# Kernel tuning notes

Measured on AMD Instinct MI355X. Metric: run time of the kernel, lower is better.

## Reference

```python
import jax, jax.numpy as jnp
import numpy as np

B, T, IN, H, L = 256, 80, 39, 256, 5


def _xavier(key, shape):
    fan_out, fan_in = shape[0], shape[1]
    std = (2.0 / (fan_in + fan_out)) ** 0.5
    return std * jax.random.normal(key, shape, dtype=jnp.float32)


def setup_inputs() -> dict:
    key = jax.random.key(0)
    ks = jax.random.split(key, 4 + 2 * L)
    x = jax.random.normal(ks[0], (B, T, IN), dtype=jnp.float32)
    # PyTorch LSTM params, gate order (i, f, g, o); biases zero per init.
    W_ih0 = _xavier(ks[1], (4 * H, IN))                       # layer 0 input weights
    W_ih_rest = jnp.stack([_xavier(ks[2 + l], (4 * H, H)) for l in range(L - 1)])  # [L-1,4H,H]
    W_hh = jnp.stack([_xavier(ks[1 + L + l], (4 * H, H)) for l in range(L)])       # [L,4H,H]
    b_ih = jnp.zeros((L, 4 * H), dtype=jnp.float32)
    b_hh = jnp.zeros((L, 4 * H), dtype=jnp.float32)
    fc_w = _xavier(ks[2 * L + 1], (1, H))
    fc_b = jnp.zeros((1,), dtype=jnp.float32)
    return {"x": x, "W_ih0": W_ih0, "W_ih_rest": W_ih_rest, "W_hh": W_hh,
            "b_ih": b_ih, "b_hh": b_hh, "fc_w": fc_w, "fc_b": fc_b}


def _lstm_layer(xs, W_ih, W_hh_l, b_ih_l, b_hh_l):
    # xs: [B,T,D]. Precompute input projection for all timesteps (one big GEMM).
    x_proj = jnp.einsum('btd,gd->btg', xs, W_ih) + b_ih_l + b_hh_l  # [B,T,4H]

    def step(carry, xp):
        h, c = carry
        gates = xp + h @ W_hh_l.T                 # [B,4H]
        i, f, g, o = jnp.split(gates, 4, axis=-1)
        c = jax.nn.sigmoid(f) * c + jax.nn.sigmoid(i) * jnp.tanh(g)
        h = jax.nn.sigmoid(o) * jnp.tanh(c)
        return (h, c), h

    b = xs.shape[0]
    h0 = jnp.zeros((b, H), dtype=xs.dtype)
    _, hs = jax.lax.scan(step, (h0, h0), jnp.swapaxes(x_proj, 0, 1))
    return jnp.swapaxes(hs, 0, 1)  # [B,T,H]


def reference(x, W_ih0, W_ih_rest, W_hh, b_ih, b_hh, fc_w, fc_b):
    h = _lstm_layer(x, W_ih0, W_hh[0], b_ih[0], b_hh[0])
    for l in range(1, L):
        h = _lstm_layer(h, W_ih_rest[l - 1], W_hh[l], b_ih[l], b_hh[l])
    out = jnp.einsum('bth,oh->bto', h, fc_w) + fc_b  # [B,T,1]
    return out[..., 0]  # [B,T]
```

## Files before the change

kernel.cpp:

```cpp
#include <hip/hip_runtime.h>

#define B_ 256
#define T_ 80
#define IN_ 39
#define H_ 256
#define G_ 1024
#define L_ 5
#define TC_ 16
#define NCH_ 5

#define XP_FLOATS   (B_ * TC_ * G_)
#define HBUF_FLOATS (B_ * T_ * H_)
#define CBUF_FLOATS (B_ * H_)
#define WG_FLOATS   (L_ * G_ * H_)
#define HX_FLOATS   (2 * 32 * 2048)
#define CNT_OFF_FLOATS (XP_FLOATS + HBUF_FLOATS + CBUF_FLOATS + WG_FLOATS + HX_FLOATS)

#define AG __HIP_MEMORY_SCOPE_AGENT

__device__ __forceinline__ float sigm(float x) { return 1.0f / (1.0f + expf(-x)); }
__device__ __forceinline__ void fma4(float4& a, float s, const float4& w) {
    a.x = fmaf(s, w.x, a.x); a.y = fmaf(s, w.y, a.y);
    a.z = fmaf(s, w.z, a.z); a.w = fmaf(s, w.w, a.w);
}
__device__ __forceinline__ void red4(float4& a) {
    a.x += __shfl_xor(a.x, 32); a.y += __shfl_xor(a.y, 32);
    a.z += __shfl_xor(a.z, 32); a.w += __shfl_xor(a.w, 32);
}
__device__ __forceinline__ float lo32(unsigned long long v) { return __uint_as_float((unsigned)v); }
__device__ __forceinline__ float hi32(unsigned long long v) { return __uint_as_float((unsigned)(v >> 32)); }

extern "C" __global__ void __launch_bounds__(256)
wt_kernel(const float* __restrict__ Whh, float* __restrict__ Wg) {
    const int gid = blockIdx.x * 256 + threadIdx.x;
    const int g4 = gid & 3;
    const int j  = (gid >> 2) & 31;
    const int k  = (gid >> 7) & 255;
    const int s  = (gid >> 15) & 7;
    const int l  = gid >> 18;
    Wg[gid] = Whh[((size_t)(l * 1024 + g4 * 256 + s * 32 + j)) * 256 + k];
}

extern "C" __global__ void __launch_bounds__(256)
proj_kernel(const float* __restrict__ src, const float* __restrict__ Wih,
            const float* __restrict__ bihl, const float* __restrict__ bhhl,
            float* __restrict__ xp, int K, int t0) {
    __shared__ float As[16 * 68];
    __shared__ float Bs[16 * 68];
    const int tid = threadIdx.x;
    const int mt = blockIdx.x >> 4, nt = blockIdx.x & 15;
    const int tx = tid & 15, ty = tid >> 4;
    const int lr = tid >> 2, lc4 = (tid & 3) << 2;

    const int ar = mt * 64 + lr;
    const int ab = ar >> 4;
    const int at = t0 + (ar & 15);
    const float* arow = src + ((size_t)ab * T_ + at) * K;
    const float* brow = Wih + (size_t)(nt * 64 + lr) * K;

    float acc[4][4];
    #pragma unroll
    for (int i = 0; i < 4; ++i)
        #pragma unroll
        for (int j = 0; j < 4; ++j) acc[i][j] = 0.0f;

    for (int k0 = 0; k0 < K; k0 += 16) {
        __syncthreads();
        if (K == IN_) {
            #pragma unroll
            for (int i = 0; i < 4; ++i) {
                int k = k0 + lc4 + i;
                As[(lc4 + i) * 68 + lr] = (k < IN_) ? arow[k] : 0.0f;
                Bs[(lc4 + i) * 68 + lr] = (k < IN_) ? brow[k] : 0.0f;
            }
        } else {
            float4 av = *(const float4*)(arow + k0 + lc4);
            float4 bv = *(const float4*)(brow + k0 + lc4);
            As[(lc4 + 0) * 68 + lr] = av.x;
            As[(lc4 + 1) * 68 + lr] = av.y;
            As[(lc4 + 2) * 68 + lr] = av.z;
            As[(lc4 + 3) * 68 + lr] = av.w;
            Bs[(lc4 + 0) * 68 + lr] = bv.x;
            Bs[(lc4 + 1) * 68 + lr] = bv.y;
            Bs[(lc4 + 2) * 68 + lr] = bv.z;
            Bs[(lc4 + 3) * 68 + lr] = bv.w;
        }
        __syncthreads();
        #pragma unroll
        for (int kk = 0; kk < 16; ++kk) {
            float4 a4 = *(const float4*)&As[kk * 68 + ty * 4];
            float4 b4 = *(const float4*)&Bs[kk * 68 + tx * 4];
            acc[0][0] += a4.x * b4.x; acc[0][1] += a4.x * b4.y;
            acc[0][2] += a4.x * b4.z; acc[0][3] += a4.x * b4.w;
            acc[1][0] += a4.y * b4.x; acc[1][1] += a4.y * b4.y;
            acc[1][2] += a4.y * b4.z; acc[1][3] += a4.y * b4.w;
            acc[2][0] += a4.z * b4.x; acc[2][1] += a4.z * b4.y;
            acc[2][2] += a4.z * b4.z; acc[2][3] += a4.z * b4.w;
            acc[3][0] += a4.w * b4.x; acc[3][1] += a4.w * b4.y;
            acc[3][2] += a4.w * b4.z; acc[3][3] += a4.w * b4.w;
        }
    }
    const int col = nt * 64 + tx * 4;
    const float bs0 = bihl[col + 0] + bhhl[col + 0];
    const float bs1 = bihl[col + 1] + bhhl[col + 1];
    const float bs2 = bihl[col + 2] + bhhl[col + 2];
    const float bs3 = bihl[col + 3] + bhhl[col + 3];
    #pragma unroll
    for (int i = 0; i < 4; ++i) {
        const int row = mt * 64 + ty * 4 + i;
        float4 o;
        o.x = acc[i][0] + bs0; o.y = acc[i][1] + bs1;
        o.z = acc[i][2] + bs2; o.w = acc[i][3] + bs3;
        *(float4*)&xp[(size_t)row * G_ + col] = o;
    }
}

extern "C" __global__ void __launch_bounds__(256, 1)
rec2_kernel(const float* __restrict__ xp, const float* __restrict__ Wg_l,
            float* __restrict__ hbuf, float* __restrict__ cbuf,
            float* __restrict__ hx, int* __restrict__ cnt,
            int t0, int chkb, int first) {
    extern __shared__ float smem[];
    float* sW = smem;
    float* sH = smem + 32768;
    float* sP = smem + 34816;

    const int tid = threadIdx.x;
    const int bid = blockIdx.x;
    const int grp = bid & 31;
    const int s   = bid >> 5;
    const int jj  = tid & 31;
    const int ks  = tid >> 5;
    const int w   = tid >> 6;
    const int fb  = tid >> 5;
    const int fj  = tid & 31;
    const int bglob = grp * 8 + fb;
    const int unit  = s * 32 + fj;
    int* cnt_g = cnt + grp * 32;

    {
        const float4* Wgs = (const float4*)Wg_l + (size_t)s * 8192;
        float4* sW4 = (float4*)sW;
        #pragma unroll 4
        for (int i = tid; i < 8192; i += 256) sW4[i] = Wgs[i];
    }

    float creg = first ? 0.0f : cbuf[(size_t)bglob * H_ + unit];
    const float4* sW4 = (const float4*)sW;

    for (int tt = 0; tt < TC_; ++tt) {
        const int t = t0 + tt;

        if (tt == 0) {
            if (first) {
                for (int i = tid; i < 2048; i += 256) sH[i] = 0.0f;
            } else {
                const int u = tid;
                #pragma unroll
                for (int bb = 0; bb < 8; ++bb)
                    sH[u * 8 + bb] = hbuf[((size_t)(grp * 8 + bb) * T_ + (t0 - 1)) * H_ + u];
            }
        } else {
            if (tid == 0) {
                const int tgt = 8 * (chkb + tt);
                while (__hip_atomic_load(cnt_g, __ATOMIC_RELAXED, AG) < tgt)
                    __builtin_amdgcn_s_sleep(1);
            }
            __syncthreads();
            const unsigned long long* hs =
                (const unsigned long long*)(hx + (size_t)(((tt - 1) & 1) * 32 + grp) * 2048);
            const int u = tid;
            unsigned long long v0 = __hip_atomic_load(hs + u * 4 + 0, __ATOMIC_RELAXED, AG);
            unsigned long long v1 = __hip_atomic_load(hs + u * 4 + 1, __ATOMIC_RELAXED, AG);
            unsigned long long v2 = __hip_atomic_load(hs + u * 4 + 2, __ATOMIC_RELAXED, AG);
            unsigned long long v3 = __hip_atomic_load(hs + u * 4 + 3, __ATOMIC_RELAXED, AG);
            float4 fa, fbv;
            fa.x = lo32(v0); fa.y = hi32(v0); fa.z = lo32(v1); fa.w = hi32(v1);
            fbv.x = lo32(v2); fbv.y = hi32(v2); fbv.z = lo32(v3); fbv.w = hi32(v3);
            *(float4*)&sH[u * 8] = fa;
            *(float4*)&sH[u * 8 + 4] = fbv;
        }

        const size_t xrow = ((size_t)bglob * TC_ + tt) * G_ + unit;
        const float x0 = xp[xrow];
        const float x1 = xp[xrow + 256];
        const float x2 = xp[xrow + 512];
        const float x3 = xp[xrow + 768];

        __syncthreads();

        float4 a0 = {0,0,0,0}, a1 = {0,0,0,0}, a2 = {0,0,0,0}, a3 = {0,0,0,0};
        float4 a4 = {0,0,0,0}, a5 = {0,0,0,0}, a6 = {0,0,0,0}, a7 = {0,0,0,0};
        #pragma unroll 4
        for (int kk = 0; kk < 32; ++kk) {
            const int k = ks * 32 + kk;
            const float4 wv = sW4[k * 32 + jj];
            const float4 ha = *(const float4*)&sH[k * 8];
            const float4 hb = *(const float4*)&sH[k * 8 + 4];
            fma4(a0, ha.x, wv); fma4(a1, ha.y, wv);
            fma4(a2, ha.z, wv); fma4(a3, ha.w, wv);
            fma4(a4, hb.x, wv); fma4(a5, hb.y, wv);
            fma4(a6, hb.z, wv); fma4(a7, hb.w, wv);
        }
        red4(a0); red4(a1); red4(a2); red4(a3);
        red4(a4); red4(a5); red4(a6); red4(a7);
        if ((tid & 63) < 32) {
            float4* pp = (float4*)&sP[(w * 32 + jj) * 36];
            pp[0] = a0; pp[1] = a1; pp[2] = a2; pp[3] = a3;
            pp[4] = a4; pp[5] = a5; pp[6] = a6; pp[7] = a7;
        }
        __syncthreads();

        float4 g4;
        g4.x = x0; g4.y = x1; g4.z = x2; g4.w = x3;
        #pragma unroll
        for (int w2 = 0; w2 < 4; ++w2) {
            const float4 pw = *(const float4*)&sP[(w2 * 32 + fj) * 36 + fb * 4];
            g4.x += pw.x; g4.y += pw.y; g4.z += pw.z; g4.w += pw.w;
        }
        const float I = sigm(g4.x);
        const float F = sigm(g4.y);
        const float Gt = tanhf(g4.z);
        const float O = sigm(g4.w);
        creg = F * creg + I * Gt;
        const float hval = O * tanhf(creg);
        hbuf[((size_t)bglob * T_ + t) * H_ + unit] = hval;

        if (tt < TC_ - 1) {
            __hip_atomic_store(hx + (size_t)((tt & 1) * 32 + grp) * 2048 + unit * 8 + fb,
                               hval, __ATOMIC_RELAXED, AG);
            asm volatile("s_waitcnt vmcnt(0)" ::: "memory");
            __syncthreads();
            if (tid == 0)
                __hip_atomic_fetch_add(cnt_g, 1, __ATOMIC_RELAXED, AG);
        }
    }

    cbuf[(size_t)bglob * H_ + unit] = creg;
}

extern "C" __global__ void __launch_bounds__(128)
fc_kernel(const float* __restrict__ hbuf, const float* __restrict__ fcw,
          const float* __restrict__ fcb, float* __restrict__ out) {
    __shared__ float wsm[256];
    const int tid = threadIdx.x;
    const int b = blockIdx.x;
    if (tid < 64) ((float4*)wsm)[tid] = ((const float4*)fcw)[tid];
    __syncthreads();
    if (tid < T_) {
        const float4* h4p = (const float4*)(hbuf + ((size_t)b * T_ + tid) * H_);
        const float4* w4p = (const float4*)wsm;
        float acc = fcb[0];
        #pragma unroll 8
        for (int k4 = 0; k4 < 64; ++k4) {
            float4 h4 = h4p[k4], w4 = w4p[k4];
            acc += h4.x * w4.x + h4.y * w4.y + h4.z * w4.z + h4.w * w4.w;
        }
        out[b * T_ + tid] = acc;
    }
}

extern "C" void kernel_launch(void* const* d_in, const int* in_sizes, int n_in,
                              void* d_out, int out_size, void* d_ws, size_t ws_size,
                              hipStream_t stream) {
    (void)in_sizes; (void)n_in; (void)out_size; (void)ws_size;
    const float* x    = (const float*)d_in[0];
    const float* Wih0 = (const float*)d_in[1];
    const float* Wihr = (const float*)d_in[2];
    const float* Whh  = (const float*)d_in[3];
    const float* bih  = (const float*)d_in[4];
    const float* bhh  = (const float*)d_in[5];
    const float* fcw  = (const float*)d_in[6];
    const float* fcb  = (const float*)d_in[7];
    float* out = (float*)d_out;
    float* ws  = (float*)d_ws;

    float* xp   = ws;
    float* hbuf = ws + XP_FLOATS;
    float* cbuf = hbuf + HBUF_FLOATS;
    float* wg   = cbuf + CBUF_FLOATS;
    float* hx   = wg + WG_FLOATS;
    int*   cnt  = (int*)(ws + CNT_OFF_FLOATS);

    hipMemsetAsync(cnt, 0, 32 * 32 * sizeof(int), stream);
    hipLaunchKernelGGL(wt_kernel, dim3(WG_FLOATS / 256), dim3(256), 0, stream, Whh, wg);

    for (int l = 0; l < L_; ++l) {
        const int K = (l == 0) ? IN_ : H_;
        const float* src = (l == 0) ? x : hbuf;
        const float* Wih = (l == 0) ? Wih0 : (Wihr + (size_t)(l - 1) * G_ * H_);
        const float* Wg_l = wg + (size_t)l * (G_ * H_);
        for (int ch = 0; ch < NCH_; ++ch) {
            const int t0 = ch * TC_;
            const int chkb = (l * NCH_ + ch) * (TC_ - 1);
            hipLaunchKernelGGL(proj_kernel, dim3(1024), dim3(256), 0, stream,
                               src, Wih, bih + l * G_, bhh + l * G_, xp, K, t0);
            hipLaunchKernelGGL(rec2_kernel, dim3(256), dim3(256), 157696, stream,
                               xp, Wg_l, hbuf, cbuf, hx, cnt, t0, chkb, ch == 0 ? 1 : 0);
        }
    }
    hipLaunchKernelGGL(fc_kernel, dim3(B_), dim3(128), 0, stream, hbuf, fcw, fcb, out);
}
```

Measured before the change: 2.688 ms.

## Replace counter barrier with tagged 64-bit h exchange slots

Each hidden value is now published as a 64-bit word that packs the float with a step tag. Consumers spin on their own 8 slots until every tag matches, instead of waiting on a per-group atomic counter. This removes the waitcnt, the extra __syncthreads and the fetch_add on the producer side, and the single-thread wait plus block barrier on the consumer side. The cost is more polling traffic, since every thread repeatedly loads 8 words, and the exchange buffer doubles in size and must be zeroed at start.

```diff
diff --git a/kernel.cpp b/kernel.cpp
--- a/kernel.cpp
+++ b/kernel.cpp
@@ -13,8 +13,8 @@
 #define HBUF_FLOATS (B_ * T_ * H_)
 #define CBUF_FLOATS (B_ * H_)
 #define WG_FLOATS   (L_ * G_ * H_)
-#define HX_FLOATS   (2 * 32 * 2048)
-#define CNT_OFF_FLOATS (XP_FLOATS + HBUF_FLOATS + CBUF_FLOATS + WG_FLOATS + HX_FLOATS)
+#define HX_U64      (2 * 32 * 2048)
+#define HX_OFF_FLOATS (XP_FLOATS + HBUF_FLOATS + CBUF_FLOATS + WG_FLOATS)
 
 #define AG __HIP_MEMORY_SCOPE_AGENT
 
@@ -27,8 +27,6 @@
     a.x += __shfl_xor(a.x, 32); a.y += __shfl_xor(a.y, 32);
     a.z += __shfl_xor(a.z, 32); a.w += __shfl_xor(a.w, 32);
 }
-__device__ __forceinline__ float lo32(unsigned long long v) { return __uint_as_float((unsigned)v); }
-__device__ __forceinline__ float hi32(unsigned long long v) { return __uint_as_float((unsigned)(v >> 32)); }
 
 extern "C" __global__ void __launch_bounds__(256)
 wt_kernel(const float* __restrict__ Whh, float* __restrict__ Wg) {
@@ -118,8 +116,8 @@
 extern "C" __global__ void __launch_bounds__(256, 1)
 rec2_kernel(const float* __restrict__ xp, const float* __restrict__ Wg_l,
             float* __restrict__ hbuf, float* __restrict__ cbuf,
-            float* __restrict__ hx, int* __restrict__ cnt,
-            int t0, int chkb, int first) {
+            unsigned long long* __restrict__ hx,
+            int t0, int tagb, int first) {
     extern __shared__ float smem[];
     float* sW = smem;
     float* sH = smem + 32768;
@@ -136,7 +134,6 @@
     const int fj  = tid & 31;
     const int bglob = grp * 8 + fb;
     const int unit  = s * 32 + fj;
-    int* cnt_g = cnt + grp * 32;
 
     {
         const float4* Wgs = (const float4*)Wg_l + (size_t)s * 8192;
@@ -161,24 +158,24 @@
                     sH[u * 8 + bb] = hbuf[((size_t)(grp * 8 + bb) * T_ + (t0 - 1)) * H_ + u];
             }
         } else {
-            if (tid == 0) {
-                const int tgt = 8 * (chkb + tt);
-                while (__hip_atomic_load(cnt_g, __ATOMIC_RELAXED, AG) < tgt)
-                    __builtin_amdgcn_s_sleep(1);
+            const unsigned exp_tag = (unsigned)(tagb + tt - 1);
+            const unsigned long long* hs =
+                hx + (size_t)(((tt - 1) & 1) * 32 + grp) * 2048 + (size_t)tid * 8;
+            unsigned long long v[8];
+            for (;;) {
+                bool ok = true;
+                #pragma unroll
+                for (int b = 0; b < 8; ++b)
+                    v[b] = __hip_atomic_load(hs + b, __ATOMIC_RELAXED, AG);
+                #pragma unroll
+                for (int b = 0; b < 8; ++b)
+                    ok = ok && ((unsigned)(v[b] >> 32) == exp_tag);
+                if (ok) break;
+                __builtin_amdgcn_s_sleep(1);
             }
-            __syncthreads();
-            const unsigned long long* hs =
-                (const unsigned long long*)(hx + (size_t)(((tt - 1) & 1) * 32 + grp) * 2048);
-            const int u = tid;
-            unsigned long long v0 = __hip_atomic_load(hs + u * 4 + 0, __ATOMIC_RELAXED, AG);
-            unsigned long long v1 = __hip_atomic_load(hs + u * 4 + 1, __ATOMIC_RELAXED, AG);
-            unsigned long long v2 = __hip_atomic_load(hs + u * 4 + 2, __ATOMIC_RELAXED, AG);
-            unsigned long long v3 = __hip_atomic_load(hs + u * 4 + 3, __ATOMIC_RELAXED, AG);
-            float4 fa, fbv;
-            fa.x = lo32(v0); fa.y = hi32(v0); fa.z = lo32(v1); fa.w = hi32(v1);
-            fbv.x = lo32(v2); fbv.y = hi32(v2); fbv.z = lo32(v3); fbv.w = hi32(v3);
-            *(float4*)&sH[u * 8] = fa;
-            *(float4*)&sH[u * 8 + 4] = fbv;
+            #pragma unroll
+            for (int b = 0; b < 8; ++b)
+                sH[tid * 8 + b] = __uint_as_float((unsigned)v[b]);
         }
 
         const size_t xrow = ((size_t)bglob * TC_ + tt) * G_ + unit;
@@ -227,12 +224,11 @@
         hbuf[((size_t)bglob * T_ + t) * H_ + unit] = hval;
 
         if (tt < TC_ - 1) {
-            __hip_atomic_store(hx + (size_t)((tt & 1) * 32 + grp) * 2048 + unit * 8 + fb,
-                               hval, __ATOMIC_RELAXED, AG);
-            asm volatile("s_waitcnt vmcnt(0)" ::: "memory");
-            __syncthreads();
-            if (tid == 0)
-                __hip_atomic_fetch_add(cnt_g, 1, __ATOMIC_RELAXED, AG);
+            const unsigned long long pv =
+                ((unsigned long long)(unsigned)(tagb + tt) << 32) | __float_as_uint(hval);
+            __hip_atomic_store(hx + (size_t)((tt & 1) * 32 + grp) * 2048
+                                  + (size_t)unit * 8 + fb,
+                               pv, __ATOMIC_RELAXED, AG);
         }
     }
 
@@ -279,10 +275,9 @@
     float* hbuf = ws + XP_FLOATS;
     float* cbuf = hbuf + HBUF_FLOATS;
     float* wg   = cbuf + CBUF_FLOATS;
-    float* hx   = wg + WG_FLOATS;
-    int*   cnt  = (int*)(ws + CNT_OFF_FLOATS);
-
-    hipMemsetAsync(cnt, 0, 32 * 32 * sizeof(int), stream);
+    unsigned long long* hx = (unsigned long long*)(ws + HX_OFF_FLOATS);
+
+    hipMemsetAsync(hx, 0, HX_U64 * sizeof(unsigned long long), stream);
     hipLaunchKernelGGL(wt_kernel, dim3(WG_FLOATS / 256), dim3(256), 0, stream, Whh, wg);
 
     for (int l = 0; l < L_; ++l) {
@@ -292,11 +287,11 @@
         const float* Wg_l = wg + (size_t)l * (G_ * H_);
         for (int ch = 0; ch < NCH_; ++ch) {
             const int t0 = ch * TC_;
-            const int chkb = (l * NCH_ + ch) * (TC_ - 1);
+            const int tagb = (l * NCH_ + ch) * TC_ + 1;
             hipLaunchKernelGGL(proj_kernel, dim3(1024), dim3(256), 0, stream,
                                src, Wih, bih + l * G_, bhh + l * G_, xp, K, t0);
             hipLaunchKernelGGL(rec2_kernel, dim3(256), dim3(256), 157696, stream,
-                               xp, Wg_l, hbuf, cbuf, hx, cnt, t0, chkb, ch == 0 ? 1 : 0);
+                               xp, Wg_l, hbuf, cbuf, hx, t0, tagb, ch == 0 ? 1 : 0);
         }
     }
     hipLaunchKernelGGL(fc_kernel, dim3(B_), dim3(128), 0, stream, hbuf, fcw, fcb, out);
```

Result: slower. 3.940 ms (+46.6%).

## Keep recurrent weights in registers with 512-thread blocks instead of LDS

Applied to the files above, without the earlier changes.

The recurrent kernel now loads each thread's slice of W_hh into 16 float4 registers instead of staging 128KB in shared memory. Block size doubles to 512 threads, so each thread covers 16 k-values, and the cross-wave partial-sum reduction widens to 8 slices. Only the first 256 threads run the gate math. The aim is to remove LDS bandwidth pressure on the weight reads in the per-step matvec and to add more waves for latency hiding. In exchange, register pressure rises and the reduction step grows.

```diff
diff --git a/kernel.cpp b/kernel.cpp
--- a/kernel.cpp
+++ b/kernel.cpp
@@ -115,15 +115,13 @@
     }
 }
 
-extern "C" __global__ void __launch_bounds__(256, 1)
-rec2_kernel(const float* __restrict__ xp, const float* __restrict__ Wg_l,
+extern "C" __global__ void __launch_bounds__(512, 2)
+rec3_kernel(const float* __restrict__ xp, const float* __restrict__ Wg_l,
             float* __restrict__ hbuf, float* __restrict__ cbuf,
             float* __restrict__ hx, int* __restrict__ cnt,
             int t0, int chkb, int first) {
-    extern __shared__ float smem[];
-    float* sW = smem;
-    float* sH = smem + 32768;
-    float* sP = smem + 34816;
+    __shared__ float sH[2048];
+    __shared__ float sP[8 * 32 * 36];
 
     const int tid = threadIdx.x;
     const int bid = blockIdx.x;
@@ -132,29 +130,30 @@
     const int jj  = tid & 31;
     const int ks  = tid >> 5;
     const int w   = tid >> 6;
-    const int fb  = tid >> 5;
+    const int fb  = (tid >> 5) & 7;
     const int fj  = tid & 31;
     const int bglob = grp * 8 + fb;
     const int unit  = s * 32 + fj;
     int* cnt_g = cnt + grp * 32;
 
-    {
-        const float4* Wgs = (const float4*)Wg_l + (size_t)s * 8192;
-        float4* sW4 = (float4*)sW;
-        #pragma unroll 4
-        for (int i = tid; i < 8192; i += 256) sW4[i] = Wgs[i];
-    }
-
-    float creg = first ? 0.0f : cbuf[(size_t)bglob * H_ + unit];
-    const float4* sW4 = (const float4*)sW;
+    const float4* Wg4 = (const float4*)Wg_l + (size_t)s * 8192;
+    float4 wreg[16];
+    #pragma unroll
+    for (int kk = 0; kk < 16; ++kk)
+        wreg[kk] = Wg4[(size_t)(ks * 16 + kk) * 32 + jj];
+
+    float creg = 0.0f;
+    if (tid < 256 && !first) creg = cbuf[(size_t)bglob * H_ + unit];
+
+    const float4* sH4 = (const float4*)sH;
 
     for (int tt = 0; tt < TC_; ++tt) {
         const int t = t0 + tt;
 
         if (tt == 0) {
             if (first) {
-                for (int i = tid; i < 2048; i += 256) sH[i] = 0.0f;
-            } else {
+                for (int i = tid; i < 2048; i += 512) sH[i] = 0.0f;
+            } else if (tid < 256) {
                 const int u = tid;
                 #pragma unroll
                 for (int bb = 0; bb < 8; ++bb)
@@ -167,36 +166,41 @@
                     __builtin_amdgcn_s_sleep(1);
             }
             __syncthreads();
-            const unsigned long long* hs =
-                (const unsigned long long*)(hx + (size_t)(((tt - 1) & 1) * 32 + grp) * 2048);
-            const int u = tid;
-            unsigned long long v0 = __hip_atomic_load(hs + u * 4 + 0, __ATOMIC_RELAXED, AG);
-            unsigned long long v1 = __hip_atomic_load(hs + u * 4 + 1, __ATOMIC_RELAXED, AG);
-            unsigned long long v2 = __hip_atomic_load(hs + u * 4 + 2, __ATOMIC_RELAXED, AG);
-            unsigned long long v3 = __hip_atomic_load(hs + u * 4 + 3, __ATOMIC_RELAXED, AG);
-            float4 fa, fbv;
-            fa.x = lo32(v0); fa.y = hi32(v0); fa.z = lo32(v1); fa.w = hi32(v1);
-            fbv.x = lo32(v2); fbv.y = hi32(v2); fbv.z = lo32(v3); fbv.w = hi32(v3);
-            *(float4*)&sH[u * 8] = fa;
-            *(float4*)&sH[u * 8 + 4] = fbv;
-        }
-
-        const size_t xrow = ((size_t)bglob * TC_ + tt) * G_ + unit;
-        const float x0 = xp[xrow];
-        const float x1 = xp[xrow + 256];
-        const float x2 = xp[xrow + 512];
-        const float x3 = xp[xrow + 768];
+            if (tid < 256) {
+                const unsigned long long* hs =
+                    (const unsigned long long*)(hx + (size_t)(((tt - 1) & 1) * 32 + grp) * 2048);
+                const int u = tid;
+                unsigned long long v0 = __hip_atomic_load(hs + u * 4 + 0, __ATOMIC_RELAXED, AG);
+                unsigned long long v1 = __hip_atomic_load(hs + u * 4 + 1, __ATOMIC_RELAXED, AG);
+                unsigned long long v2 = __hip_atomic_load(hs + u * 4 + 2, __ATOMIC_RELAXED, AG);
+                unsigned long long v3 = __hip_atomic_load(hs + u * 4 + 3, __ATOMIC_RELAXED, AG);
+                float4 fa, fbv;
+                fa.x = lo32(v0); fa.y = hi32(v0); fa.z = lo32(v1); fa.w = hi32(v1);
+                fbv.x = lo32(v2); fbv.y = hi32(v2); fbv.z = lo32(v3); fbv.w = hi32(v3);
+                *(float4*)&sH[u * 8] = fa;
+                *(float4*)&sH[u * 8 + 4] = fbv;
+            }
+        }
+
+        float x0 = 0.f, x1 = 0.f, x2 = 0.f, x3 = 0.f;
+        if (tid < 256) {
+            const size_t xrow = ((size_t)bglob * TC_ + tt) * G_ + unit;
+            x0 = xp[xrow];
+            x1 = xp[xrow + 256];
+            x2 = xp[xrow + 512];
+            x3 = xp[xrow + 768];
+        }
 
         __syncthreads();
 
         float4 a0 = {0,0,0,0}, a1 = {0,0,0,0}, a2 = {0,0,0,0}, a3 = {0,0,0,0};
         float4 a4 = {0,0,0,0}, a5 = {0,0,0,0}, a6 = {0,0,0,0}, a7 = {0,0,0,0};
-        #pragma unroll 4
-        for (int kk = 0; kk < 32; ++kk) {
-            const int k = ks * 32 + kk;
-            const float4 wv = sW4[k * 32 + jj];
-            const float4 ha = *(const float4*)&sH[k * 8];
-            const float4 hb = *(const float4*)&sH[k * 8 + 4];
+        #pragma unroll
+        for (int kk = 0; kk < 16; ++kk) {
+            const int k = ks * 16 + kk;
+            const float4 wv = wreg[kk];
+            const float4 ha = sH4[k * 2];
+            const float4 hb = sH4[k * 2 + 1];
             fma4(a0, ha.x, wv); fma4(a1, ha.y, wv);
             fma4(a2, ha.z, wv); fma4(a3, ha.w, wv);
             fma4(a4, hb.x, wv); fma4(a5, hb.y, wv);
@@ -211,24 +215,29 @@
         }
         __syncthreads();
 
-        float4 g4;
-        g4.x = x0; g4.y = x1; g4.z = x2; g4.w = x3;
-        #pragma unroll
-        for (int w2 = 0; w2 < 4; ++w2) {
-            const float4 pw = *(const float4*)&sP[(w2 * 32 + fj) * 36 + fb * 4];
-            g4.x += pw.x; g4.y += pw.y; g4.z += pw.z; g4.w += pw.w;
-        }
-        const float I = sigm(g4.x);
-        const float F = sigm(g4.y);
-        const float Gt = tanhf(g4.z);
-        const float O = sigm(g4.w);
-        creg = F * creg + I * Gt;
-        const float hval = O * tanhf(creg);
-        hbuf[((size_t)bglob * T_ + t) * H_ + unit] = hval;
+        if (tid < 256) {
+            float4 g4;
+            g4.x = x0; g4.y = x1; g4.z = x2; g4.w = x3;
+            #pragma unroll
+            for (int w2 = 0; w2 < 8; ++w2) {
+                const float4 pw = *(const float4*)&sP[(w2 * 32 + fj) * 36 + fb * 4];
+                g4.x += pw.x; g4.y += pw.y; g4.z += pw.z; g4.w += pw.w;
+            }
+            const float I = sigm(g4.x);
+            const float F = sigm(g4.y);
+            const float Gt = tanhf(g4.z);
+            const float O = sigm(g4.w);
+            creg = F * creg + I * Gt;
+            const float hval = O * tanhf(creg);
+            hbuf[((size_t)bglob * T_ + t) * H_ + unit] = hval;
+
+            if (tt < TC_ - 1) {
+                __hip_atomic_store(hx + (size_t)((tt & 1) * 32 + grp) * 2048 + unit * 8 + fb,
+                                   hval, __ATOMIC_RELAXED, AG);
+            }
+        }
 
         if (tt < TC_ - 1) {
-            __hip_atomic_store(hx + (size_t)((tt & 1) * 32 + grp) * 2048 + unit * 8 + fb,
-                               hval, __ATOMIC_RELAXED, AG);
             asm volatile("s_waitcnt vmcnt(0)" ::: "memory");
             __syncthreads();
             if (tid == 0)
@@ -236,7 +245,7 @@
         }
     }
 
-    cbuf[(size_t)bglob * H_ + unit] = creg;
+    if (tid < 256) cbuf[(size_t)bglob * H_ + unit] = creg;
 }
 
 extern "C" __global__ void __launch_bounds__(128)
@@ -295,7 +304,7 @@
             const int chkb = (l * NCH_ + ch) * (TC_ - 1);
             hipLaunchKernelGGL(proj_kernel, dim3(1024), dim3(256), 0, stream,
                                src, Wih, bih + l * G_, bhh + l * G_, xp, K, t0);
-            hipLaunchKernelGGL(rec2_kernel, dim3(256), dim3(256), 157696, stream,
+            hipLaunchKernelGGL(rec3_kernel, dim3(256), dim3(512), 0, stream,
                                xp, Wg_l, hbuf, cbuf, hx, cnt, t0, chkb, ch == 0 ? 1 : 0);
         }
     }
```

After: 2.604 ms. 3.1% less time.
